# Kernel tuning notes

Measured on AMD Instinct MI355X. Metric: run time of the kernel, lower is better.

Reference implementation:

```python
import jax, jax.numpy as jnp
import numpy as np

B, NV, RN, SN = 1, 4, 1024, 128
H = W = 256
C_FEAT = 32   # img_feat_dim
D_VIEW = 32   # view transformer d_model
PE_D = 8      # PE_d_hid
D_RAY = D_VIEW + PE_D  # 40
NHEAD = 8
EPS_LN = 1e-5


def _layernorm(x, g, b):
    m = x.mean(-1, keepdims=True)
    v = ((x - m) ** 2).mean(-1, keepdims=True)
    return (x - m) * jax.lax.rsqrt(v + EPS_LN) * g + b


def _linear_attention(q, k, v):
    # LoFTR kernelized linear attention; q,k,v: (n, L, h, d)
    Q = jax.nn.elu(q) + 1.0
    K = jax.nn.elu(k) + 1.0
    L = v.shape[1]
    KV = jnp.einsum('nshd,nshv->nhdv', K, v / L)
    Z = 1.0 / (jnp.einsum('nlhd,nhd->nlh', Q, K.sum(axis=1)) + 1e-6)
    return jnp.einsum('nlhd,nhdv,nlh->nlhv', Q, KV, Z) * L


def _loftr_self_layer(x, Wq, Wk, Wv, Wm, g1, b1, W1, W2, g2, b2):
    # LoFTREncoderLayer with self-attention (x is both query and source)
    n, L, d = x.shape
    dim = d // NHEAD
    q = (x @ Wq).reshape(n, L, NHEAD, dim)
    k = (x @ Wk).reshape(n, L, NHEAD, dim)
    v = (x @ Wv).reshape(n, L, NHEAD, dim)
    msg = _linear_attention(q, k, v).reshape(n, L, d) @ Wm
    msg = _layernorm(msg, g1, b1)
    msg = jax.nn.relu(jnp.concatenate([x, msg], -1) @ W1) @ W2
    msg = _layernorm(msg, g2, b2)
    return x + msg


def _grid_sample_2d(img, pix):
    # img: (N,C,H,W); pix: (N,RN,SN,2) in pixel coords.
    # bilinear, align_corners=True, zero padding; mask = in-bounds.
    N, C, Hh, Ww = img.shape
    x, y = pix[..., 0], pix[..., 1]
    mask = ((x >= 0) & (x <= Ww - 1) & (y >= 0) & (y <= Hh - 1)).astype(img.dtype)
    x0 = jnp.floor(x)
    y0 = jnp.floor(y)
    flat = img.reshape(N, C, Hh * Ww)

    def gather(ix, iy):
        valid = ((ix >= 0) & (ix < Ww) & (iy >= 0) & (iy < Hh)).astype(img.dtype)
        idx = (jnp.clip(iy, 0, Hh - 1) * Ww + jnp.clip(ix, 0, Ww - 1)).astype(jnp.int32)
        out = jnp.take_along_axis(flat, idx.reshape(N, 1, -1), axis=2)
        return out.reshape(N, C, ix.shape[1], ix.shape[2]) * valid[:, None]

    wx1 = x - x0
    wy1 = y - y0
    out = (gather(x0, y0) * ((1 - wx1) * (1 - wy1))[:, None]
           + gather(x0 + 1, y0) * (wx1 * (1 - wy1))[:, None]
           + gather(x0, y0 + 1) * ((1 - wx1) * wy1)[:, None]
           + gather(x0 + 1, y0 + 1) * (wx1 * wy1)[:, None])
    return out, mask


def _order_posenc(d_hid, n):
    pos = np.arange(n)[:, None].astype(np.float64)
    j = np.arange(d_hid)[None, :]
    tab = pos / np.power(10000.0, 2 * (j // 2) / d_hid)
    tab[:, 0::2] = np.sin(tab[:, 0::2])
    tab[:, 1::2] = np.cos(tab[:, 1::2])
    return jnp.asarray(tab, dtype=jnp.float32)


def _forward(point3D, source_imgs, source_imgs_feat, ref_pose_inv, source_poses_inv,
             source_poses, view_token,
             vt_Wq, vt_Wk, vt_Wv, vt_Wm, vt_g1, vt_b1, vt_W1, vt_W2, vt_g2, vt_b2,
             rt_Wq, rt_Wk, rt_Wv, rt_Wm, rt_g1, rt_b1, rt_W1, rt_W2, rt_g2, rt_b2,
             dm_W1, dm_b1, dm_W2, dm_b2, dm_W3, dm_b3,
             rw_W1, rw_b1, rw_W2, rw_b2, rw_W3, rw_b3):
    b, nv, _, h, w = source_imgs.shape
    _, rn, sn, _ = point3D.shape

    # relative viewing directions (B,NV,RN,SN,3)
    v1 = point3D - ref_pose_inv[:, None, None, :3, -1]
    v2 = point3D[:, None] - source_poses_inv[:, :, None, None, :3, -1]
    v1 = v1 / jnp.linalg.norm(v1, axis=-1, keepdims=True)
    v2 = v2 / jnp.linalg.norm(v2, axis=-1, keepdims=True)
    dir_relative = v1[:, None] - v2

    # project points into all source views: (B,NV,3,RN,SN)
    pts_h = jnp.concatenate([point3D, jnp.ones_like(point3D[..., :1])], -1)
    pip = jnp.einsum('bnij,brsj->bnirs', source_poses, pts_h)[:, :, :3]
    mask_valid_depth = (pip[:, :, 2] > 0).astype(point3D.dtype)
    pix = pip[:, :, :2] / pip[:, :, 2:3]
    grid = jnp.moveaxis(pix, 2, -1).reshape(b * nv, rn, sn, 2)

    feat_s, mask = _grid_sample_2d(source_imgs_feat.reshape(b * nv, -1, h, w), grid)
    rgb_s, _ = _grid_sample_2d(source_imgs.reshape(b * nv, -1, h, w), grid)
    mask = mask.reshape(b, nv, rn, sn) * mask_valid_depth

    # per-point multi-view tokens: (B*RN*SN, NV, C)
    x = feat_s.reshape(b, nv, -1, rn, sn).transpose(0, 3, 4, 1, 2).reshape(b * rn * sn, nv, -1)
    tok = jnp.broadcast_to(view_token, (x.shape[0], 1, view_token.shape[-1]))
    x = jnp.concatenate([tok, x], axis=1)  # prepend view token -> L = NV+1
    x = _loftr_self_layer(x, vt_Wq, vt_Wk, vt_Wv, vt_Wm, vt_g1, vt_b1, vt_W1, vt_W2, vt_g2, vt_b2)

    x1 = jnp.moveaxis(x, 1, 0)          # (NV+1, B*RN*SN, C)
    view_feature = x1[1:]
    x = x1[0].reshape(b * rn, sn, -1)   # token output per sample along ray

    pe = _order_posenc(PE_D, sn)        # (SN, 8)
    x = jnp.concatenate([x, jnp.broadcast_to(pe, (b * rn, sn, PE_D))], -1)
    x = _loftr_self_layer(x, rt_Wq, rt_Wk, rt_Wv, rt_Wm, rt_g1, rt_b1, rt_W1, rt_W2, rt_g2, rt_b2)

    hdm = jax.nn.relu(x @ dm_W1 + dm_b1)
    hdm = jax.nn.relu(hdm @ dm_W2 + dm_b2)
    srdf = hdm @ dm_W3 + dm_b3           # (B*RN, SN, 1)

    # radiance blending weights over views
    vf = view_feature.reshape(nv, b, rn, sn, -1).transpose(1, 2, 3, 0, 4)  # (B,RN,SN,NV,C)
    dr = dir_relative.transpose(0, 2, 3, 1, 4)                             # (B,RN,SN,NV,3)
    xw = jnp.concatenate([vf, dr], -1)
    xw = jax.nn.relu(xw @ rw_W1 + rw_b1)
    xw = jax.nn.relu(xw @ rw_W2 + rw_b2)
    xw = xw @ rw_W3 + rw_b3                                                # (B,RN,SN,NV,1)
    m = mask.transpose(0, 2, 3, 1)[..., None]
    xw = jnp.where(m == 0, -1e9, xw)
    weight = jax.nn.softmax(xw, axis=-2)
    w_bn = weight[..., 0].transpose(0, 3, 1, 2)[:, :, None]                # (B,NV,1,RN,SN)
    radiance = (rgb_s.reshape(b, nv, 3, rn, sn) * w_bn).sum(axis=1)        # (B,3,RN,SN)
    radiance = radiance.transpose(0, 2, 3, 1).reshape(b * rn * sn, 3)
    return radiance, srdf, pip


def setup_inputs() -> dict:
    key = jax.random.key(0)
    ks = jax.random.split(key, 4)
    u = jax.random.uniform(ks[0], (B, RN, SN, 3), dtype=jnp.float32)
    point3D = jnp.concatenate([u[..., :2] - 0.5, u[..., 2:] + 1.0], -1)  # x,y in [-.5,.5], z in [1,2]
    source_imgs = jax.random.normal(ks[1], (B, NV, 3, H, W), dtype=jnp.float32) * 0.5
    source_imgs_feat = jax.random.normal(ks[2], (B, NV, C_FEAT, H, W), dtype=jnp.float32) * 0.5

    f = 200.0
    P = np.array([[f, 0, W / 2, 0], [0, f, H / 2, 0], [0, 0, 1, 0], [0, 0, 0, 1]], np.float32)
    source_poses = jnp.asarray(np.broadcast_to(P, (B, NV, 4, 4)).copy())
    ref_pose_inv = jnp.asarray(np.broadcast_to(np.eye(4, dtype=np.float32), (B, 4, 4)).copy())
    spi = np.broadcast_to(np.eye(4, dtype=np.float32), (B, NV, 4, 4)).copy()
    spi[:, :, 0, 3] = np.linspace(-0.2, 0.2, NV, dtype=np.float32)  # camera centers
    source_poses_inv = jnp.asarray(spi)

    pk = jax.random.split(ks[3], 20)

    def lin(k, i, o):
        return jax.random.normal(k, (i, o), dtype=jnp.float32) * 0.05

    d, dr = D_VIEW, D_RAY
    params = dict(
        view_token=jax.random.normal(pk[0], (1, d), dtype=jnp.float32),
        vt_Wq=lin(pk[1], d, d), vt_Wk=lin(pk[2], d, d), vt_Wv=lin(pk[3], d, d), vt_Wm=lin(pk[4], d, d),
        vt_g1=jnp.ones(d), vt_b1=jnp.zeros(d),
        vt_W1=lin(pk[5], 2 * d, 2 * d), vt_W2=lin(pk[6], 2 * d, d),
        vt_g2=jnp.ones(d), vt_b2=jnp.zeros(d),
        rt_Wq=lin(pk[7], dr, dr), rt_Wk=lin(pk[8], dr, dr), rt_Wv=lin(pk[9], dr, dr), rt_Wm=lin(pk[10], dr, dr),
        rt_g1=jnp.ones(dr), rt_b1=jnp.zeros(dr),
        rt_W1=lin(pk[11], 2 * dr, 2 * dr), rt_W2=lin(pk[12], 2 * dr, dr),
        rt_g2=jnp.ones(dr), rt_b2=jnp.zeros(dr),
        dm_W1=lin(pk[13], dr, 32), dm_b1=jnp.zeros(32),
        dm_W2=lin(pk[14], 32, 16), dm_b2=jnp.zeros(16),
        dm_W3=lin(pk[15], 16, 1), dm_b3=jnp.zeros(1),
        rw_W1=lin(pk[16], d + 3, 16), rw_b1=jnp.zeros(16),
        rw_W2=lin(pk[17], 16, 8), rw_b2=jnp.zeros(8),
        rw_W3=lin(pk[18], 8, 1), rw_b3=jnp.zeros(1),
    )
    out = dict(point3D=point3D, source_imgs=source_imgs, source_imgs_feat=source_imgs_feat,
               ref_pose_inv=ref_pose_inv, source_poses_inv=source_poses_inv,
               source_poses=source_poses)
    out.update(params)
    return out


def reference(point3D, source_imgs, source_imgs_feat, ref_pose_inv, source_poses_inv,
              source_poses, view_token,
              vt_Wq, vt_Wk, vt_Wv, vt_Wm, vt_g1, vt_b1, vt_W1, vt_W2, vt_g2, vt_b2,
              rt_Wq, rt_Wk, rt_Wv, rt_Wm, rt_g1, rt_b1, rt_W1, rt_W2, rt_g2, rt_b2,
              dm_W1, dm_b1, dm_W2, dm_b2, dm_W3, dm_b3,
              rw_W1, rw_b1, rw_W2, rw_b2, rw_W3, rw_b3):
    return _forward(point3D, source_imgs, source_imgs_feat, ref_pose_inv, source_poses_inv,
                    source_poses, view_token,
                    vt_Wq, vt_Wk, vt_Wv, vt_Wm, vt_g1, vt_b1, vt_W1, vt_W2, vt_g2, vt_b2,
                    rt_Wq, rt_Wk, rt_Wv, rt_Wm, rt_g1, rt_b1, rt_W1, rt_W2, rt_g2, rt_b2,
                    dm_W1, dm_b1, dm_W2, dm_b2, dm_W3, dm_b3,
                    rw_W1, rw_b1, rw_W2, rw_b2, rw_W3, rw_b3)
```

## Files before the change

### kernel.cpp

```cpp
#include <hip/hip_runtime.h>
#include <math.h>

#define NPTS   131072
#define NVIEW  4
#define IMH    256
#define IMW    256

#define WS_FEATT   0u
#define WS_IMGT    8388608u
#define WS_X1      9437184u
#define WS_XR      26214400u
#define WS_MSG     31457280u
#define WS_RGB     36700160u
#define WS_DIR     38273024u
#define WS_MASK    39845888u

__device__ __forceinline__ float elup1(float t) { return t > 0.f ? t + 1.f : expf(t); }

__global__ __launch_bounds__(256) void k0_transpose(
    const float* __restrict__ feat, const float* __restrict__ img,
    float* __restrict__ featT, float* __restrict__ imgT)
{
    int tid = blockIdx.x * 256 + threadIdx.x;
    int v = tid >> 16, pix = tid & 65535;
    float buf[32];
#pragma unroll
    for (int c = 0; c < 32; ++c)
        buf[c] = feat[((size_t)(v * 32 + c) << 16) + pix];
    float4* dst = (float4*)(featT + ((size_t)tid << 5));
#pragma unroll
    for (int q = 0; q < 8; ++q)
        dst[q] = make_float4(buf[4*q], buf[4*q+1], buf[4*q+2], buf[4*q+3]);
    float4 rgb;
    rgb.x = img[((size_t)(v * 3 + 0) << 16) + pix];
    rgb.y = img[((size_t)(v * 3 + 1) << 16) + pix];
    rgb.z = img[((size_t)(v * 3 + 2) << 16) + pix];
    rgb.w = 0.f;
    *(float4*)(imgT + ((size_t)tid << 2)) = rgb;
}

__global__ __launch_bounds__(256) void k1_geom_sample(
    const float* __restrict__ p3d, const float* __restrict__ rpi,
    const float* __restrict__ spi, const float* __restrict__ sp,
    const float* __restrict__ featT, const float* __restrict__ imgT,
    float* __restrict__ x1, float* __restrict__ rgbw,
    float* __restrict__ dirw, float* __restrict__ maskw,
    float* __restrict__ outpip)
{
    int tid = blockIdx.x * 256 + threadIdx.x;
    int p = tid >> 2, v = tid & 3;
    float X = p3d[p * 3 + 0], Y = p3d[p * 3 + 1], Z = p3d[p * 3 + 2];

    float a0 = X - rpi[3], a1 = Y - rpi[7], a2 = Z - rpi[11];
    float na = sqrtf(a0 * a0 + a1 * a1 + a2 * a2);
    a0 /= na; a1 /= na; a2 /= na;
    const float* sv = spi + v * 16;
    float b0 = X - sv[3], b1 = Y - sv[7], b2 = Z - sv[11];
    float nb = sqrtf(b0 * b0 + b1 * b1 + b2 * b2);
    b0 /= nb; b1 /= nb; b2 /= nb;
    dirw[(size_t)p * 12 + v * 3 + 0] = a0 - b0;
    dirw[(size_t)p * 12 + v * 3 + 1] = a1 - b1;
    dirw[(size_t)p * 12 + v * 3 + 2] = a2 - b2;

    const float* P = sp + v * 16;
    float pip0 = P[0] * X + P[1] * Y + P[2]  * Z + P[3];
    float pip1 = P[4] * X + P[5] * Y + P[6]  * Z + P[7];
    float pip2 = P[8] * X + P[9] * Y + P[10] * Z + P[11];
    outpip[(size_t)(v * 3 + 0) * NPTS + p] = pip0;
    outpip[(size_t)(v * 3 + 1) * NPTS + p] = pip1;
    outpip[(size_t)(v * 3 + 2) * NPTS + p] = pip2;

    float gx = pip0 / pip2, gy = pip1 / pip2;
    float inb = (gx >= 0.f && gx <= 255.f && gy >= 0.f && gy <= 255.f) ? 1.f : 0.f;
    float mvd = pip2 > 0.f ? 1.f : 0.f;
    maskw[(size_t)p * 4 + v] = inb * mvd;

    float x0f = floorf(gx), y0f = floorf(gy);
    float wx = gx - x0f, wy = gy - y0f;
    int ix0 = (int)x0f, iy0 = (int)y0f;
    float tw[4] = { (1.f-wx)*(1.f-wy), wx*(1.f-wy), (1.f-wx)*wy, wx*wy };
    int tdx[4] = { 0, 1, 0, 1 };
    int tdy[4] = { 0, 0, 1, 1 };

    float facc[32];
#pragma unroll
    for (int c = 0; c < 32; ++c) facc[c] = 0.f;
    float r0 = 0.f, r1 = 0.f, r2 = 0.f;

#pragma unroll
    for (int tno = 0; tno < 4; ++tno) {
        int ix = ix0 + tdx[tno], iy = iy0 + tdy[tno];
        float valid = (ix >= 0 && ix < IMW && iy >= 0 && iy < IMH) ? 1.f : 0.f;
        int cx = min(max(ix, 0), IMW - 1), cy = min(max(iy, 0), IMH - 1);
        float wgt = tw[tno] * valid;
        size_t base = ((size_t)v << 16) + ((size_t)cy << 8) + (size_t)cx;
        const float4* fp = (const float4*)(featT + base * 32);
#pragma unroll
        for (int q = 0; q < 8; ++q) {
            float4 f4 = fp[q];
            facc[4*q+0] += f4.x * wgt; facc[4*q+1] += f4.y * wgt;
            facc[4*q+2] += f4.z * wgt; facc[4*q+3] += f4.w * wgt;
        }
        float4 rp = *(const float4*)(imgT + base * 4);
        r0 += rp.x * wgt; r1 += rp.y * wgt; r2 += rp.z * wgt;
    }

    float4* xd = (float4*)(x1 + ((size_t)p * 4 + v) * 32);
#pragma unroll
    for (int q = 0; q < 8; ++q)
        xd[q] = make_float4(facc[4*q], facc[4*q+1], facc[4*q+2], facc[4*q+3]);
    rgbw[(size_t)p * 12 + v * 3 + 0] = r0;
    rgbw[(size_t)p * 12 + v * 3 + 1] = r1;
    rgbw[(size_t)p * 12 + v * 3 + 2] = r2;
}

#define K2_BLK    128
#define K2_PTS    24
#define K2_GRID   1024
#define K2_NGRP   ((NPTS + K2_PTS - 1) / K2_PTS)

__device__ __forceinline__ void fma4(const float4 xv, const float* __restrict__ w,
                                     const int stride, float* __restrict__ acc)
{
#pragma unroll
    for (int j = 0; j < 32; ++j) acc[j] = fmaf(xv.x, w[j],            acc[j]);
#pragma unroll
    for (int j = 0; j < 32; ++j) acc[j] = fmaf(xv.y, w[stride + j],   acc[j]);
#pragma unroll
    for (int j = 0; j < 32; ++j) acc[j] = fmaf(xv.z, w[2*stride + j], acc[j]);
#pragma unroll
    for (int j = 0; j < 32; ++j) acc[j] = fmaf(xv.w, w[3*stride + j], acc[j]);
}

__device__ __forceinline__ void fma40(const float4 xv, const float* __restrict__ w,
                                      const int stride, float* __restrict__ acc)
{
#pragma unroll
    for (int j = 0; j < 40; ++j) acc[j] = fmaf(xv.x, w[j],            acc[j]);
#pragma unroll
    for (int j = 0; j < 40; ++j) acc[j] = fmaf(xv.y, w[stride + j],   acc[j]);
#pragma unroll
    for (int j = 0; j < 40; ++j) acc[j] = fmaf(xv.z, w[2*stride + j], acc[j]);
#pragma unroll
    for (int j = 0; j < 40; ++j) acc[j] = fmaf(xv.w, w[3*stride + j], acc[j]);
}

__global__ __launch_bounds__(K2_BLK) void k2_loftr1(
    float* __restrict__ x1g, const float* __restrict__ vtok,
    const float* __restrict__ Wq, const float* __restrict__ Wk,
    const float* __restrict__ Wv, const float* __restrict__ Wm,
    const float* __restrict__ g1v, const float* __restrict__ b1v,
    const float* __restrict__ W1, const float* __restrict__ W2,
    const float* __restrict__ g2v, const float* __restrict__ b2v,
    float* __restrict__ xr)
{
    __shared__ float shr[8192];

    int t = threadIdx.x;
    int pl = t / 5, l = t - pl * 5;
    bool act = (t < K2_PTS * 5);
    if (!act) { pl = 0; l = 0; }
    const int rowbase = (pl * 5 + l) * 68;

    for (int grp = blockIdx.x; grp < K2_NGRP; grp += gridDim.x) {
        int p = grp * K2_PTS + pl;
        bool valid = act && (p < NPTS);
        int pload = p < NPTS ? p : NPTS - 1;
        const float4* xsrc = (l == 0) ? (const float4*)vtok
                                      : (const float4*)(x1g + ((size_t)pload * 4 + (l - 1)) * 32);

        __syncthreads();

        {
            float acc[32];
#pragma unroll
            for (int j = 0; j < 32; ++j) acc[j] = 0.f;
            for (int g = 0; g < 8; ++g) {
                float4 xv = xsrc[g];
                fma4(xv, &Wk[g * 128], 32, acc);
            }
            if (act) {
                float* krow = &shr[rowbase];
#pragma unroll
                for (int j = 0; j < 32; j += 4)
                    *(float4*)&krow[j] = make_float4(elup1(acc[j]), elup1(acc[j+1]),
                                                     elup1(acc[j+2]), elup1(acc[j+3]));
            }
        }
        {
            float acc[32];
#pragma unroll
            for (int j = 0; j < 32; ++j) acc[j] = 0.f;
            for (int g = 0; g < 8; ++g) {
                float4 xv = xsrc[g];
                fma4(xv, &Wv[g * 128], 32, acc);
            }
            if (act) {
                float* vrow = &shr[rowbase + 32];
#pragma unroll
                for (int j = 0; j < 32; j += 4)
                    *(float4*)&vrow[j] = make_float4(acc[j], acc[j+1], acc[j+2], acc[j+3]);
            }
        }
        __syncthreads();

        float macc[32];
#pragma unroll
        for (int j = 0; j < 32; ++j) macc[j] = 0.f;
        for (int h = 0; h < 8; ++h) {
            float q0 = 0.f, q1 = 0.f, q2 = 0.f, q3 = 0.f;
            for (int g = 0; g < 8; ++g) {
                float4 xv = xsrc[g];
                const float* w = &Wq[g * 128 + h * 4];
                q0 = fmaf(xv.x, w[0],  q0); q1 = fmaf(xv.x, w[1],  q1);
                q2 = fmaf(xv.x, w[2],  q2); q3 = fmaf(xv.x, w[3],  q3);
                q0 = fmaf(xv.y, w[32], q0); q1 = fmaf(xv.y, w[33], q1);
                q2 = fmaf(xv.y, w[34], q2); q3 = fmaf(xv.y, w[35], q3);
                q0 = fmaf(xv.z, w[64], q0); q1 = fmaf(xv.z, w[65], q1);
                q2 = fmaf(xv.z, w[66], q2); q3 = fmaf(xv.z, w[67], q3);
                q0 = fmaf(xv.w, w[96], q0); q1 = fmaf(xv.w, w[97], q1);
                q2 = fmaf(xv.w, w[98], q2); q3 = fmaf(xv.w, w[99], q3);
            }
            q0 = elup1(q0); q1 = elup1(q1); q2 = elup1(q2); q3 = elup1(q3);

            float kvm[16] = {0,0,0,0,0,0,0,0,0,0,0,0,0,0,0,0};
            float ks0 = 0.f, ks1 = 0.f, ks2 = 0.f, ks3 = 0.f;
#pragma unroll
            for (int l2 = 0; l2 < 5; ++l2) {
                const float* row = &shr[(pl * 5 + l2) * 68 + h * 4];
                float4 K4 = *(const float4*)row;
                float4 V4 = *(const float4*)(row + 32);
                kvm[0]  = fmaf(K4.x, V4.x, kvm[0]);  kvm[1]  = fmaf(K4.x, V4.y, kvm[1]);
                kvm[2]  = fmaf(K4.x, V4.z, kvm[2]);  kvm[3]  = fmaf(K4.x, V4.w, kvm[3]);
                kvm[4]  = fmaf(K4.y, V4.x, kvm[4]);  kvm[5]  = fmaf(K4.y, V4.y, kvm[5]);
                kvm[6]  = fmaf(K4.y, V4.z, kvm[6]);  kvm[7]  = fmaf(K4.y, V4.w, kvm[7]);
                kvm[8]  = fmaf(K4.z, V4.x, kvm[8]);  kvm[9]  = fmaf(K4.z, V4.y, kvm[9]);
                kvm[10] = fmaf(K4.z, V4.z, kvm[10]); kvm[11] = fmaf(K4.z, V4.w, kvm[11]);
                kvm[12] = fmaf(K4.w, V4.x, kvm[12]); kvm[13] = fmaf(K4.w, V4.y, kvm[13]);
                kvm[14] = fmaf(K4.w, V4.z, kvm[14]); kvm[15] = fmaf(K4.w, V4.w, kvm[15]);
                ks0 += K4.x; ks1 += K4.y; ks2 += K4.z; ks3 += K4.w;
            }
            float den = 1e-6f + q0*ks0 + q1*ks1 + q2*ks2 + q3*ks3;
            float inv = 1.f / den;
            float o0 = (q0*kvm[0] + q1*kvm[4] + q2*kvm[8]  + q3*kvm[12]) * inv;
            float o1 = (q0*kvm[1] + q1*kvm[5] + q2*kvm[9]  + q3*kvm[13]) * inv;
            float o2 = (q0*kvm[2] + q1*kvm[6] + q2*kvm[10] + q3*kvm[14]) * inv;
            float o3 = (q0*kvm[3] + q1*kvm[7] + q2*kvm[11] + q3*kvm[15]) * inv;

            const float* wm = &Wm[h * 4 * 32];
#pragma unroll
            for (int j = 0; j < 32; ++j) macc[j] = fmaf(o0, wm[j],      macc[j]);
#pragma unroll
            for (int j = 0; j < 32; ++j) macc[j] = fmaf(o1, wm[32 + j], macc[j]);
#pragma unroll
            for (int j = 0; j < 32; ++j) macc[j] = fmaf(o2, wm[64 + j], macc[j]);
#pragma unroll
            for (int j = 0; j < 32; ++j) macc[j] = fmaf(o3, wm[96 + j], macc[j]);
        }

        float msg[32];
        {
            float s1 = 0.f, s2 = 0.f;
#pragma unroll
            for (int j = 0; j < 32; ++j) { s1 += macc[j]; s2 += macc[j] * macc[j]; }
            float m  = s1 * (1.f / 32.f);
            float va = s2 * (1.f / 32.f) - m * m;
            float rs = rsqrtf(va + 1e-5f);
#pragma unroll
            for (int j = 0; j < 32; ++j)
                msg[j] = (macc[j] - m) * rs * g1v[j] + b1v[j];
        }
        __syncthreads();

#pragma unroll
        for (int g = 0; g < 8; ++g)
            *(float4*)&shr[(g * K2_BLK + t) * 4] =
                make_float4(msg[4*g], msg[4*g+1], msg[4*g+2], msg[4*g+3]);

        float oacc[32];
#pragma unroll
        for (int j = 0; j < 32; ++j) oacc[j] = 0.f;
        for (int half = 0; half < 2; ++half) {
            const int j0 = half * 32;
            float hacc[32];
#pragma unroll
            for (int j = 0; j < 32; ++j) hacc[j] = 0.f;
            for (int g = 0; g < 8; ++g) {
                float4 xv = xsrc[g];
                fma4(xv, &W1[(g * 4) * 64 + j0], 64, hacc);
            }
            for (int g = 0; g < 8; ++g) {
                float4 mv = *(const float4*)&shr[(g * K2_BLK + t) * 4];
                fma4(mv, &W1[(32 + g * 4) * 64 + j0], 64, hacc);
            }
#pragma unroll
            for (int j = 0; j < 32; j += 4)
                *(float4*)&shr[4096 + ((j >> 2) * K2_BLK + t) * 4] =
                    make_float4(fmaxf(hacc[j], 0.f),   fmaxf(hacc[j+1], 0.f),
                                fmaxf(hacc[j+2], 0.f), fmaxf(hacc[j+3], 0.f));
            for (int g = 0; g < 8; ++g) {
                float4 hv = *(const float4*)&shr[4096 + (g * K2_BLK + t) * 4];
                fma4(hv, &W2[(j0 + g * 4) * 32], 32, oacc);
            }
        }

        {
            float s1 = 0.f, s2 = 0.f;
#pragma unroll
            for (int j = 0; j < 32; ++j) { s1 += oacc[j]; s2 += oacc[j] * oacc[j]; }
            float m  = s1 * (1.f / 32.f);
            float va = s2 * (1.f / 32.f) - m * m;
            float rs = rsqrtf(va + 1e-5f);

            if (valid) {
                float y[32];
#pragma unroll
                for (int g = 0; g < 8; ++g) {
                    float4 x4 = xsrc[g];
                    y[4*g] = x4.x; y[4*g+1] = x4.y; y[4*g+2] = x4.z; y[4*g+3] = x4.w;
                }
#pragma unroll
                for (int j = 0; j < 32; ++j)
                    y[j] += (oacc[j] - m) * rs * g2v[j] + b2v[j];

                if (l == 0) {
                    float4* dst = (float4*)(xr + (size_t)p * 40);
#pragma unroll
                    for (int g = 0; g < 8; ++g)
                        dst[g] = make_float4(y[4*g], y[4*g+1], y[4*g+2], y[4*g+3]);
                    int sidx = p & 127;
#pragma unroll
                    for (int c = 0; c < 8; ++c) {
                        float den = (c < 2) ? 1.f : (c < 4) ? 10.f : (c < 6) ? 100.f : 1000.f;
                        float arg = (float)sidx / den;
                        xr[(size_t)p * 40 + 32 + c] = (c & 1) ? cosf(arg) : sinf(arg);
                    }
                } else {
                    float4* dst = (float4*)(x1g + ((size_t)p * 4 + (l - 1)) * 32);
#pragma unroll
                    for (int g = 0; g < 8; ++g)
                        dst[g] = make_float4(y[4*g], y[4*g+1], y[4*g+2], y[4*g+3]);
                }
            }
        }
    }
}

#define KT_STRIDE 132
__global__ __launch_bounds__(128) void k3a_attn(
    const float* __restrict__ xr,
    const float* __restrict__ Wq, const float* __restrict__ Wk,
    const float* __restrict__ Wv, const float* __restrict__ Wm,
    const float* __restrict__ g1, const float* __restrict__ b1,
    float* __restrict__ msg)
{
    __shared__ float KT[40 * KT_STRIDE];
    __shared__ float VT[40 * KT_STRIDE];
    __shared__ float kvb[200];
    __shared__ float ksb[40];

    int t = threadIdx.x, r = blockIdx.x;
    const float4* x4 = (const float4*)(xr + ((size_t)r * 128 + t) * 40);

    {
        float acc[40];
#pragma unroll
        for (int j = 0; j < 40; ++j) acc[j] = 0.f;
        for (int g = 0; g < 10; ++g)
            fma40(x4[g], &Wk[g * 160], 40, acc);
#pragma unroll
        for (int j = 0; j < 40; ++j) KT[j * KT_STRIDE + t] = elup1(acc[j]);
    }
    {
        float acc[40];
#pragma unroll
        for (int j = 0; j < 40; ++j) acc[j] = 0.f;
        for (int g = 0; g < 10; ++g)
            fma40(x4[g], &Wv[g * 160], 40, acc);
#pragma unroll
        for (int j = 0; j < 40; ++j) VT[j * KT_STRIDE + t] = acc[j];
    }
    __syncthreads();

    {
        int lane = t & 63, wid = t >> 6;
        if (lane < 20) {
            int idx = wid * 20 + lane;
            int h = idx / 5;
            float ks = 0.f;
            float kv0 = 0.f, kv1 = 0.f, kv2 = 0.f, kv3 = 0.f, kv4 = 0.f;
            const float* kr = &KT[idx * KT_STRIDE];
            const float* v0 = &VT[(h * 5 + 0) * KT_STRIDE];
            const float* v1 = &VT[(h * 5 + 1) * KT_STRIDE];
            const float* v2 = &VT[(h * 5 + 2) * KT_STRIDE];
            const float* v3 = &VT[(h * 5 + 3) * KT_STRIDE];
            const float* v4 = &VT[(h * 5 + 4) * KT_STRIDE];
            for (int s = 0; s < 128; s += 4) {
                float4 K4 = *(const float4*)&kr[s];
                float4 A = *(const float4*)&v0[s];
                float4 B = *(const float4*)&v1[s];
                float4 C = *(const float4*)&v2[s];
                float4 D = *(const float4*)&v3[s];
                float4 E = *(const float4*)&v4[s];
                ks  += K4.x + K4.y + K4.z + K4.w;
                kv0 += K4.x*A.x + K4.y*A.y + K4.z*A.z + K4.w*A.w;
                kv1 += K4.x*B.x + K4.y*B.y + K4.z*B.z + K4.w*B.w;
                kv2 += K4.x*C.x + K4.y*C.y + K4.z*C.z + K4.w*C.w;
                kv3 += K4.x*D.x + K4.y*D.y + K4.z*D.z + K4.w*D.w;
                kv4 += K4.x*E.x + K4.y*E.y + K4.z*E.z + K4.w*E.w;
            }
            ksb[idx] = ks;
            kvb[idx * 5 + 0] = kv0; kvb[idx * 5 + 1] = kv1;
            kvb[idx * 5 + 2] = kv2; kvb[idx * 5 + 3] = kv3;
            kvb[idx * 5 + 4] = kv4;
        }
    }
    __syncthreads();

    float o[40];
    {
        float q[40];
#pragma unroll
        for (int j = 0; j < 40; ++j) q[j] = 0.f;
        for (int g = 0; g < 10; ++g)
            fma40(x4[g], &Wq[g * 160], 40, q);
#pragma unroll
        for (int j = 0; j < 40; ++j) q[j] = elup1(q[j]);

#pragma unroll
        for (int h = 0; h < 8; ++h) {
            float den = 1e-6f;
#pragma unroll
            for (int e = 0; e < 5; ++e) den += q[h*5+e] * ksb[h*5+e];
            float inv = 1.f / den;
#pragma unroll
            for (int d = 0; d < 5; ++d) {
                float val = 0.f;
#pragma unroll
                for (int e = 0; e < 5; ++e)
                    val += q[h*5+e] * kvb[(h*5+e)*5 + d];
                o[h*5+d] = val * inv;
            }
        }
    }
    float macc[40];
#pragma unroll
    for (int j = 0; j < 40; ++j) macc[j] = 0.f;
#pragma unroll
    for (int g = 0; g < 10; ++g) {
        float4 ov = make_float4(o[4*g], o[4*g+1], o[4*g+2], o[4*g+3]);
        fma40(ov, &Wm[g * 160], 40, macc);
    }
    {
        float s1 = 0.f, s2 = 0.f;
#pragma unroll
        for (int j = 0; j < 40; ++j) { s1 += macc[j]; s2 += macc[j] * macc[j]; }
        float mu = s1 * (1.f / 40.f);
        float va = s2 * (1.f / 40.f) - mu * mu;
        float rs = rsqrtf(va + 1e-5f);
#pragma unroll
        for (int j = 0; j < 40; ++j)
            macc[j] = (macc[j] - mu) * rs * g1[j] + b1[j];
    }
    float4* md = (float4*)(msg + ((size_t)r * 128 + t) * 40);
#pragma unroll
    for (int g = 0; g < 10; ++g)
        md[g] = make_float4(macc[4*g], macc[4*g+1], macc[4*g+2], macc[4*g+3]);
}

__global__ __launch_bounds__(128) void k3b_ffn(
    float* __restrict__ xr, const float* __restrict__ msg,
    const float* __restrict__ W1, const float* __restrict__ W2,
    const float* __restrict__ g2, const float* __restrict__ b2)
{
    int p = blockIdx.x * 128 + threadIdx.x;
    const float4* x4 = (const float4*)(xr + (size_t)p * 40);
    const float4* m4 = (const float4*)(msg + (size_t)p * 40);

    float oacc[40];
#pragma unroll
    for (int j = 0; j < 40; ++j) oacc[j] = 0.f;

#pragma unroll
    for (int half = 0; half < 2; ++half) {
        const int j0 = half * 40;
        float hacc[40];
#pragma unroll
        for (int j = 0; j < 40; ++j) hacc[j] = 0.f;
        for (int g = 0; g < 10; ++g)
            fma40(x4[g], &W1[(g * 4) * 80 + j0], 80, hacc);
        for (int g = 0; g < 10; ++g)
            fma40(m4[g], &W1[(40 + g * 4) * 80 + j0], 80, hacc);
#pragma unroll
        for (int j = 0; j < 40; ++j) hacc[j] = fmaxf(hacc[j], 0.f);
#pragma unroll
        for (int g = 0; g < 10; ++g) {
            float4 hv = make_float4(hacc[4*g], hacc[4*g+1], hacc[4*g+2], hacc[4*g+3]);
            fma40(hv, &W2[(j0 + g * 4) * 40], 40, oacc);
        }
    }

    float s1 = 0.f, s2 = 0.f;
#pragma unroll
    for (int j = 0; j < 40; ++j) { s1 += oacc[j]; s2 += oacc[j] * oacc[j]; }
    float mu = s1 * (1.f / 40.f);
    float va = s2 * (1.f / 40.f) - mu * mu;
    float rs = rsqrtf(va + 1e-5f);

    float4* dst = (float4*)(xr + (size_t)p * 40);
#pragma unroll
    for (int g = 0; g < 10; ++g) {
        float4 xv = x4[g];
        float4 o4;
        o4.x = xv.x + (oacc[4*g+0] - mu) * rs * g2[4*g+0] + b2[4*g+0];
        o4.y = xv.y + (oacc[4*g+1] - mu) * rs * g2[4*g+1] + b2[4*g+1];
        o4.z = xv.z + (oacc[4*g+2] - mu) * rs * g2[4*g+2] + b2[4*g+2];
        o4.w = xv.w + (oacc[4*g+3] - mu) * rs * g2[4*g+3] + b2[4*g+3];
        dst[g] = o4;
    }
}

__global__ __launch_bounds__(256) void k4_dm(
    const float* __restrict__ xr,
    const float* __restrict__ W1, const float* __restrict__ b1,
    const float* __restrict__ W2, const float* __restrict__ b2,
    const float* __restrict__ W3, const float* __restrict__ b3,
    float* __restrict__ out1)
{
    __shared__ float s[1857];
    int t = threadIdx.x;
    for (int i = t; i < 1280; i += 256) s[i] = W1[i];
    if (t < 32) s[1280 + t] = b1[t];
    for (int i = t; i < 512; i += 256) s[1312 + i] = W2[i];
    if (t < 16) { s[1824 + t] = b2[t]; s[1840 + t] = W3[t]; }
    if (t == 0) s[1856] = b3[0];
    __syncthreads();

    int p = blockIdx.x * 256 + t;
    float x[40];
    const float4* xp = (const float4*)(xr + (size_t)p * 40);
#pragma unroll
    for (int i = 0; i < 10; ++i) {
        float4 v4 = xp[i];
        x[4*i] = v4.x; x[4*i+1] = v4.y; x[4*i+2] = v4.z; x[4*i+3] = v4.w;
    }
    float h1[32];
#pragma unroll
    for (int j = 0; j < 32; ++j) h1[j] = s[1280 + j];
    for (int k = 0; k < 40; ++k) {
        float xv = x[k];
#pragma unroll
        for (int j = 0; j < 32; ++j) h1[j] += xv * s[k * 32 + j];
    }
#pragma unroll
    for (int j = 0; j < 32; ++j) h1[j] = fmaxf(h1[j], 0.f);
    float h2[16];
#pragma unroll
    for (int j = 0; j < 16; ++j) h2[j] = s[1824 + j];
    for (int k = 0; k < 32; ++k) {
        float hv = h1[k];
#pragma unroll
        for (int j = 0; j < 16; ++j) h2[j] += hv * s[1312 + k * 16 + j];
    }
    float o = s[1856];
#pragma unroll
    for (int j = 0; j < 16; ++j) o += fmaxf(h2[j], 0.f) * s[1840 + j];
    out1[p] = o;
}

__global__ __launch_bounds__(256) void k5_rw(
    const float* __restrict__ vf, const float* __restrict__ dirw,
    const float* __restrict__ maskw, const float* __restrict__ rgbw,
    const float* __restrict__ W1, const float* __restrict__ b1,
    const float* __restrict__ W2, const float* __restrict__ b2,
    const float* __restrict__ W3, const float* __restrict__ b3,
    float* __restrict__ out0)
{
    __shared__ float s[721];
    int t = threadIdx.x;
    for (int i = t; i < 560; i += 256) s[i] = W1[i];
    if (t < 16) s[560 + t] = b1[t];
    if (t < 128) s[576 + t] = W2[t];
    if (t < 8) { s[704 + t] = b2[t]; s[712 + t] = W3[t]; }
    if (t == 0) s[720] = b3[0];
    __syncthreads();

    int p = blockIdx.x * 256 + t;
    float xw[4];
#pragma unroll
    for (int v = 0; v < 4; ++v) {
        float in[35];
        const float4* vp = (const float4*)(vf + ((size_t)p * 4 + v) * 32);
#pragma unroll
        for (int q = 0; q < 8; ++q) {
            float4 f4 = vp[q];
            in[4*q] = f4.x; in[4*q+1] = f4.y; in[4*q+2] = f4.z; in[4*q+3] = f4.w;
        }
        in[32] = dirw[(size_t)p * 12 + v * 3 + 0];
        in[33] = dirw[(size_t)p * 12 + v * 3 + 1];
        in[34] = dirw[(size_t)p * 12 + v * 3 + 2];
        float h1[16];
#pragma unroll
        for (int j = 0; j < 16; ++j) h1[j] = s[560 + j];
        for (int k = 0; k < 35; ++k) {
            float xv = in[k];
#pragma unroll
            for (int j = 0; j < 16; ++j) h1[j] += xv * s[k * 16 + j];
        }
        float h2[8];
#pragma unroll
        for (int j = 0; j < 8; ++j) h2[j] = s[704 + j];
        for (int k = 0; k < 16; ++k) {
            float hv = fmaxf(h1[k], 0.f);
#pragma unroll
            for (int j = 0; j < 8; ++j) h2[j] += hv * s[576 + k * 8 + j];
        }
        float o = s[720];
#pragma unroll
        for (int j = 0; j < 8; ++j) o += fmaxf(h2[j], 0.f) * s[712 + j];
        xw[v] = (maskw[(size_t)p * 4 + v] == 0.f) ? -1e9f : o;
    }
    float m = fmaxf(fmaxf(xw[0], xw[1]), fmaxf(xw[2], xw[3]));
    float e0 = expf(xw[0] - m), e1 = expf(xw[1] - m), e2 = expf(xw[2] - m), e3 = expf(xw[3] - m);
    float inv = 1.f / (e0 + e1 + e2 + e3);
    float w4[4] = { e0 * inv, e1 * inv, e2 * inv, e3 * inv };
    float r0 = 0.f, r1 = 0.f, r2 = 0.f;
#pragma unroll
    for (int v = 0; v < 4; ++v) {
        r0 += rgbw[(size_t)p * 12 + v * 3 + 0] * w4[v];
        r1 += rgbw[(size_t)p * 12 + v * 3 + 1] * w4[v];
        r2 += rgbw[(size_t)p * 12 + v * 3 + 2] * w4[v];
    }
    out0[(size_t)p * 3 + 0] = r0;
    out0[(size_t)p * 3 + 1] = r1;
    out0[(size_t)p * 3 + 2] = r2;
}

extern "C" void kernel_launch(void* const* d_in, const int* in_sizes, int n_in,
                              void* d_out, int out_size, void* d_ws, size_t ws_size,
                              hipStream_t stream) {
    (void)in_sizes; (void)n_in; (void)out_size; (void)ws_size;
    const float* p3d   = (const float*)d_in[0];
    const float* imgs  = (const float*)d_in[1];
    const float* feat  = (const float*)d_in[2];
    const float* rpi   = (const float*)d_in[3];
    const float* spi   = (const float*)d_in[4];
    const float* sp    = (const float*)d_in[5];
    const float* vtok  = (const float*)d_in[6];
    const float* vtWq  = (const float*)d_in[7];
    const float* vtWk  = (const float*)d_in[8];
    const float* vtWv  = (const float*)d_in[9];
    const float* vtWm  = (const float*)d_in[10];
    const float* vtg1  = (const float*)d_in[11];
    const float* vtb1  = (const float*)d_in[12];
    const float* vtW1  = (const float*)d_in[13];
    const float* vtW2  = (const float*)d_in[14];
    const float* vtg2  = (const float*)d_in[15];
    const float* vtb2  = (const float*)d_in[16];
    const float* rtWq  = (const float*)d_in[17];
    const float* rtWk  = (const float*)d_in[18];
    const float* rtWv  = (const float*)d_in[19];
    const float* rtWm  = (const float*)d_in[20];
    const float* rtg1  = (const float*)d_in[21];
    const float* rtb1  = (const float*)d_in[22];
    const float* rtW1  = (const float*)d_in[23];
    const float* rtW2  = (const float*)d_in[24];
    const float* rtg2  = (const float*)d_in[25];
    const float* rtb2  = (const float*)d_in[26];
    const float* dmW1  = (const float*)d_in[27];
    const float* dmb1  = (const float*)d_in[28];
    const float* dmW2  = (const float*)d_in[29];
    const float* dmb2  = (const float*)d_in[30];
    const float* dmW3  = (const float*)d_in[31];
    const float* dmb3  = (const float*)d_in[32];
    const float* rwW1  = (const float*)d_in[33];
    const float* rwb1  = (const float*)d_in[34];
    const float* rwW2  = (const float*)d_in[35];
    const float* rwb2  = (const float*)d_in[36];
    const float* rwW3  = (const float*)d_in[37];
    const float* rwb3  = (const float*)d_in[38];

    float* out  = (float*)d_out;
    float* out0 = out;
    float* out1 = out + 393216;
    float* out2 = out + 524288;

    float* ws    = (float*)d_ws;
    float* featT = ws + WS_FEATT;
    float* imgT  = ws + WS_IMGT;
    float* x1    = ws + WS_X1;
    float* xr    = ws + WS_XR;
    float* msg   = ws + WS_MSG;
    float* rgbw  = ws + WS_RGB;
    float* dirw  = ws + WS_DIR;
    float* maskw = ws + WS_MASK;

    k0_transpose<<<dim3(1024), dim3(256), 0, stream>>>(feat, imgs, featT, imgT);
    k1_geom_sample<<<dim3(2048), dim3(256), 0, stream>>>(p3d, rpi, spi, sp, featT, imgT,
                                                         x1, rgbw, dirw, maskw, out2);
    k2_loftr1<<<dim3(K2_GRID), dim3(K2_BLK), 0, stream>>>(x1, vtok, vtWq, vtWk, vtWv, vtWm,
                                                    vtg1, vtb1, vtW1, vtW2, vtg2, vtb2, xr);
    k3a_attn<<<dim3(1024), dim3(128), 0, stream>>>(xr, rtWq, rtWk, rtWv, rtWm, rtg1, rtb1, msg);
    k3b_ffn<<<dim3(1024), dim3(128), 0, stream>>>(xr, msg, rtW1, rtW2, rtg2, rtb2);
    k4_dm<<<dim3(512), dim3(256), 0, stream>>>(xr, dmW1, dmb1, dmW2, dmb2, dmW3, dmb3, out1);
    k5_rw<<<dim3(512), dim3(256), 0, stream>>>(x1, dirw, maskw, rgbw,
                                               rwW1, rwb1, rwW2, rwb2, rwW3, rwb3, out0);
}
```

Measured before the change: 1.010 ms.

## Keep LoFTR MLP intermediates in registers, shrink LDS, fully unroll inner loops

In the view-transformer kernel, the layernormed message and hidden activations now stay in registers instead of going through shared memory. The FFN is computed in four 16-wide hidden chunks, and the shared buffer is sized to the K/V rows only, which can allow more resident blocks. Many inner loops across several kernels get full unroll pragmas, and the first kernel's grid size is raised. The trade-off is higher register pressure and code size from the unrolling and in-register hidden chunks, which could cause spills or lower occupancy.

```diff
diff --git a/kernel.cpp b/kernel.cpp
--- a/kernel.cpp
+++ b/kernel.cpp
@@ -114,36 +114,49 @@
     rgbw[(size_t)p * 12 + v * 3 + 2] = r2;
 }
 
+__device__ __forceinline__ void fma4(const float4 xv, const float* __restrict__ w,
+                                     const int stride, float* __restrict__ acc)
+{
+#pragma unroll
+    for (int j = 0; j < 32; ++j) acc[j] = fmaf(xv.x, w[j],            acc[j]);
+#pragma unroll
+    for (int j = 0; j < 32; ++j) acc[j] = fmaf(xv.y, w[stride + j],   acc[j]);
+#pragma unroll
+    for (int j = 0; j < 32; ++j) acc[j] = fmaf(xv.z, w[2*stride + j], acc[j]);
+#pragma unroll
+    for (int j = 0; j < 32; ++j) acc[j] = fmaf(xv.w, w[3*stride + j], acc[j]);
+}
+
+__device__ __forceinline__ void fma16(const float4 xv, const float* __restrict__ w,
+                                      const int stride, float* __restrict__ acc)
+{
+#pragma unroll
+    for (int j = 0; j < 16; ++j) acc[j] = fmaf(xv.x, w[j],            acc[j]);
+#pragma unroll
+    for (int j = 0; j < 16; ++j) acc[j] = fmaf(xv.y, w[stride + j],   acc[j]);
+#pragma unroll
+    for (int j = 0; j < 16; ++j) acc[j] = fmaf(xv.z, w[2*stride + j], acc[j]);
+#pragma unroll
+    for (int j = 0; j < 16; ++j) acc[j] = fmaf(xv.w, w[3*stride + j], acc[j]);
+}
+
+__device__ __forceinline__ void fma40(const float4 xv, const float* __restrict__ w,
+                                      const int stride, float* __restrict__ acc)
+{
+#pragma unroll
+    for (int j = 0; j < 40; ++j) acc[j] = fmaf(xv.x, w[j],            acc[j]);
+#pragma unroll
+    for (int j = 0; j < 40; ++j) acc[j] = fmaf(xv.y, w[stride + j],   acc[j]);
+#pragma unroll
+    for (int j = 0; j < 40; ++j) acc[j] = fmaf(xv.z, w[2*stride + j], acc[j]);
+#pragma unroll
+    for (int j = 0; j < 40; ++j) acc[j] = fmaf(xv.w, w[3*stride + j], acc[j]);
+}
+
 #define K2_BLK    128
 #define K2_PTS    24
-#define K2_GRID   1024
+#define K2_GRID   1280
 #define K2_NGRP   ((NPTS + K2_PTS - 1) / K2_PTS)
-
-__device__ __forceinline__ void fma4(const float4 xv, const float* __restrict__ w,
-                                     const int stride, float* __restrict__ acc)
-{
-#pragma unroll
-    for (int j = 0; j < 32; ++j) acc[j] = fmaf(xv.x, w[j],            acc[j]);
-#pragma unroll
-    for (int j = 0; j < 32; ++j) acc[j] = fmaf(xv.y, w[stride + j],   acc[j]);
-#pragma unroll
-    for (int j = 0; j < 32; ++j) acc[j] = fmaf(xv.z, w[2*stride + j], acc[j]);
-#pragma unroll
-    for (int j = 0; j < 32; ++j) acc[j] = fmaf(xv.w, w[3*stride + j], acc[j]);
-}
-
-__device__ __forceinline__ void fma40(const float4 xv, const float* __restrict__ w,
-                                      const int stride, float* __restrict__ acc)
-{
-#pragma unroll
-    for (int j = 0; j < 40; ++j) acc[j] = fmaf(xv.x, w[j],            acc[j]);
-#pragma unroll
-    for (int j = 0; j < 40; ++j) acc[j] = fmaf(xv.y, w[stride + j],   acc[j]);
-#pragma unroll
-    for (int j = 0; j < 40; ++j) acc[j] = fmaf(xv.z, w[2*stride + j], acc[j]);
-#pragma unroll
-    for (int j = 0; j < 40; ++j) acc[j] = fmaf(xv.w, w[3*stride + j], acc[j]);
-}
 
 __global__ __launch_bounds__(K2_BLK) void k2_loftr1(
     float* __restrict__ x1g, const float* __restrict__ vtok,
@@ -154,7 +167,7 @@
     const float* __restrict__ g2v, const float* __restrict__ b2v,
     float* __restrict__ xr)
 {
-    __shared__ float shr[8192];
+    __shared__ float shr[K2_PTS * 5 * 68];
 
     int t = threadIdx.x;
     int pl = t / 5, l = t - pl * 5;
@@ -175,6 +188,7 @@
             float acc[32];
 #pragma unroll
             for (int j = 0; j < 32; ++j) acc[j] = 0.f;
+#pragma unroll
             for (int g = 0; g < 8; ++g) {
                 float4 xv = xsrc[g];
                 fma4(xv, &Wk[g * 128], 32, acc);
@@ -191,6 +205,7 @@
             float acc[32];
 #pragma unroll
             for (int j = 0; j < 32; ++j) acc[j] = 0.f;
+#pragma unroll
             for (int g = 0; g < 8; ++g) {
                 float4 xv = xsrc[g];
                 fma4(xv, &Wv[g * 128], 32, acc);
@@ -209,6 +224,7 @@
         for (int j = 0; j < 32; ++j) macc[j] = 0.f;
         for (int h = 0; h < 8; ++h) {
             float q0 = 0.f, q1 = 0.f, q2 = 0.f, q3 = 0.f;
+#pragma unroll
             for (int g = 0; g < 8; ++g) {
                 float4 xv = xsrc[g];
                 const float* w = &Wq[g * 128 + h * 4];
@@ -258,7 +274,6 @@
             for (int j = 0; j < 32; ++j) macc[j] = fmaf(o3, wm[96 + j], macc[j]);
         }
 
-        float msg[32];
         {
             float s1 = 0.f, s2 = 0.f;
 #pragma unroll
@@ -268,39 +283,34 @@
             float rs = rsqrtf(va + 1e-5f);
 #pragma unroll
             for (int j = 0; j < 32; ++j)
-                msg[j] = (macc[j] - m) * rs * g1v[j] + b1v[j];
-        }
-        __syncthreads();
-
-#pragma unroll
-        for (int g = 0; g < 8; ++g)
-            *(float4*)&shr[(g * K2_BLK + t) * 4] =
-                make_float4(msg[4*g], msg[4*g+1], msg[4*g+2], msg[4*g+3]);
+                macc[j] = (macc[j] - m) * rs * g1v[j] + b1v[j];
+        }
 
         float oacc[32];
 #pragma unroll
         for (int j = 0; j < 32; ++j) oacc[j] = 0.f;
-        for (int half = 0; half < 2; ++half) {
-            const int j0 = half * 32;
-            float hacc[32];
-#pragma unroll
-            for (int j = 0; j < 32; ++j) hacc[j] = 0.f;
+#pragma unroll
+        for (int qq = 0; qq < 4; ++qq) {
+            const int j0 = qq * 16;
+            float hacc[16];
+#pragma unroll
+            for (int j = 0; j < 16; ++j) hacc[j] = 0.f;
+#pragma unroll
             for (int g = 0; g < 8; ++g) {
                 float4 xv = xsrc[g];
-                fma4(xv, &W1[(g * 4) * 64 + j0], 64, hacc);
-            }
+                fma16(xv, &W1[(g * 4) * 64 + j0], 64, hacc);
+            }
+#pragma unroll
             for (int g = 0; g < 8; ++g) {
-                float4 mv = *(const float4*)&shr[(g * K2_BLK + t) * 4];
-                fma4(mv, &W1[(32 + g * 4) * 64 + j0], 64, hacc);
-            }
-#pragma unroll
-            for (int j = 0; j < 32; j += 4)
-                *(float4*)&shr[4096 + ((j >> 2) * K2_BLK + t) * 4] =
-                    make_float4(fmaxf(hacc[j], 0.f),   fmaxf(hacc[j+1], 0.f),
-                                fmaxf(hacc[j+2], 0.f), fmaxf(hacc[j+3], 0.f));
-            for (int g = 0; g < 8; ++g) {
-                float4 hv = *(const float4*)&shr[4096 + (g * K2_BLK + t) * 4];
-                fma4(hv, &W2[(j0 + g * 4) * 32], 32, oacc);
+                float4 mv = make_float4(macc[4*g], macc[4*g+1], macc[4*g+2], macc[4*g+3]);
+                fma16(mv, &W1[(32 + g * 4) * 64 + j0], 64, hacc);
+            }
+#pragma unroll
+            for (int j = 0; j < 16; ++j) hacc[j] = fmaxf(hacc[j], 0.f);
+#pragma unroll
+            for (int u = 0; u < 4; ++u) {
+                float4 hv = make_float4(hacc[4*u], hacc[4*u+1], hacc[4*u+2], hacc[4*u+3]);
+                fma4(hv, &W2[(j0 + u * 4) * 32], 32, oacc);
             }
         }
 
@@ -313,21 +323,19 @@
             float rs = rsqrtf(va + 1e-5f);
 
             if (valid) {
-                float y[32];
+                float4* dst = (l == 0) ? (float4*)(xr + (size_t)p * 40)
+                                       : (float4*)(x1g + ((size_t)p * 4 + (l - 1)) * 32);
 #pragma unroll
                 for (int g = 0; g < 8; ++g) {
                     float4 x4 = xsrc[g];
-                    y[4*g] = x4.x; y[4*g+1] = x4.y; y[4*g+2] = x4.z; y[4*g+3] = x4.w;
+                    float4 o4;
+                    o4.x = x4.x + (oacc[4*g+0] - m) * rs * g2v[4*g+0] + b2v[4*g+0];
+                    o4.y = x4.y + (oacc[4*g+1] - m) * rs * g2v[4*g+1] + b2v[4*g+1];
+                    o4.z = x4.z + (oacc[4*g+2] - m) * rs * g2v[4*g+2] + b2v[4*g+2];
+                    o4.w = x4.w + (oacc[4*g+3] - m) * rs * g2v[4*g+3] + b2v[4*g+3];
+                    dst[g] = o4;
                 }
-#pragma unroll
-                for (int j = 0; j < 32; ++j)
-                    y[j] += (oacc[j] - m) * rs * g2v[j] + b2v[j];
-
                 if (l == 0) {
-                    float4* dst = (float4*)(xr + (size_t)p * 40);
-#pragma unroll
-                    for (int g = 0; g < 8; ++g)
-                        dst[g] = make_float4(y[4*g], y[4*g+1], y[4*g+2], y[4*g+3]);
                     int sidx = p & 127;
 #pragma unroll
                     for (int c = 0; c < 8; ++c) {
@@ -335,11 +343,6 @@
                         float arg = (float)sidx / den;
                         xr[(size_t)p * 40 + 32 + c] = (c & 1) ? cosf(arg) : sinf(arg);
                     }
-                } else {
-                    float4* dst = (float4*)(x1g + ((size_t)p * 4 + (l - 1)) * 32);
-#pragma unroll
-                    for (int g = 0; g < 8; ++g)
-                        dst[g] = make_float4(y[4*g], y[4*g+1], y[4*g+2], y[4*g+3]);
                 }
             }
         }
@@ -366,6 +369,7 @@
         float acc[40];
 #pragma unroll
         for (int j = 0; j < 40; ++j) acc[j] = 0.f;
+#pragma unroll
         for (int g = 0; g < 10; ++g)
             fma40(x4[g], &Wk[g * 160], 40, acc);
 #pragma unroll
@@ -375,6 +379,7 @@
         float acc[40];
 #pragma unroll
         for (int j = 0; j < 40; ++j) acc[j] = 0.f;
+#pragma unroll
         for (int g = 0; g < 10; ++g)
             fma40(x4[g], &Wv[g * 160], 40, acc);
 #pragma unroll
@@ -422,6 +427,7 @@
         float q[40];
 #pragma unroll
         for (int j = 0; j < 40; ++j) q[j] = 0.f;
+#pragma unroll
         for (int g = 0; g < 10; ++g)
             fma40(x4[g], &Wq[g * 160], 40, q);
 #pragma unroll
@@ -487,8 +493,10 @@
         float hacc[40];
 #pragma unroll
         for (int j = 0; j < 40; ++j) hacc[j] = 0.f;
+#pragma unroll
         for (int g = 0; g < 10; ++g)
             fma40(x4[g], &W1[(g * 4) * 80 + j0], 80, hacc);
+#pragma unroll
         for (int g = 0; g < 10; ++g)
             fma40(m4[g], &W1[(40 + g * 4) * 80 + j0], 80, hacc);
 #pragma unroll
@@ -547,6 +555,7 @@
     float h1[32];
 #pragma unroll
     for (int j = 0; j < 32; ++j) h1[j] = s[1280 + j];
+#pragma unroll
     for (int k = 0; k < 40; ++k) {
         float xv = x[k];
 #pragma unroll
@@ -557,6 +566,7 @@
     float h2[16];
 #pragma unroll
     for (int j = 0; j < 16; ++j) h2[j] = s[1824 + j];
+#pragma unroll
     for (int k = 0; k < 32; ++k) {
         float hv = h1[k];
 #pragma unroll
@@ -602,6 +612,7 @@
         float h1[16];
 #pragma unroll
         for (int j = 0; j < 16; ++j) h1[j] = s[560 + j];
+#pragma unroll
         for (int k = 0; k < 35; ++k) {
             float xv = in[k];
 #pragma unroll
@@ -610,6 +621,7 @@
         float h2[8];
 #pragma unroll
         for (int j = 0; j < 8; ++j) h2[j] = s[704 + j];
+#pragma unroll
         for (int k = 0; k < 16; ++k) {
             float hv = fmaxf(h1[k], 0.f);
 #pragma unroll
```

Result: slower. 1.564 ms (+54.8%).
